# Kernel tuning notes

Hardware: AMD Instinct MI355X
Metric: run time of the kernel (lower is better)

The kernel has to match this reference:

```python
import jax, jax.numpy as jnp
import numpy as np

B = 512; NPG = 50; N = B * NPG          # graphs, nodes per graph, total nodes
EPG = 100; E = B * EPG                   # edges per graph, total edges
SPG = 5; S = B * SPG                     # stems per graph, total stems
DIM = 64; FEAT = 24
CONV_STEPS = 12; S2S_STEPS = 3; NSTEM = 105

lrelu = jax.nn.leaky_relu  # negative_slope 0.01, matches nn.LeakyReLU default

def _lin(k, o, i):
    s = 1.0 / np.sqrt(i)
    return jax.random.uniform(k, (o, i), jnp.float32, -s, s)

def _vec(k, o, i):
    s = 1.0 / np.sqrt(i)
    return jax.random.uniform(k, (o,), jnp.float32, -s, s)

def setup_inputs():
    ks = jax.random.split(jax.random.key(0), 30)
    x = jax.random.normal(ks[0], (N, FEAT), jnp.float32)
    edge_attr = jax.random.uniform(ks[1], (E, 4), jnp.float32)
    gid = jnp.arange(E) // EPG
    src = gid * NPG + jax.random.randint(ks[2], (E,), 0, NPG)
    dst = gid * NPG + jax.random.randint(ks[3], (E,), 0, NPG)
    edge_index = jnp.stack([src, dst]).astype(jnp.int32)
    batch = (jnp.arange(N) // NPG).astype(jnp.int32)
    stems = jax.random.randint(ks[4], (S,), 0, NPG).astype(jnp.int32)
    stems_batch = (jnp.arange(S) // SPG).astype(jnp.int32)
    p = dict(
        lin0_w=_lin(ks[5], DIM, FEAT), lin0_b=_vec(ks[6], DIM, FEAT),
        net1_w=_lin(ks[7], 128, 4), net1_b=_vec(ks[8], 128, 4),
        net2_w=_lin(ks[9], DIM * DIM, 128), net2_b=_vec(ks[10], DIM * DIM, 128),
        root_w=_lin(ks[11], DIM, DIM), conv_b=_vec(ks[12], DIM, DIM),
        gru_wih=_lin(ks[13], 3 * DIM, DIM), gru_whh=_lin(ks[14], 3 * DIM, DIM),
        gru_bih=_vec(ks[15], 3 * DIM, DIM), gru_bhh=_vec(ks[16], 3 * DIM, DIM),
        lin1_w=_lin(ks[17], 8 * DIM, DIM), lin1_b=_vec(ks[18], 8 * DIM, DIM),
        lin2_w=_lin(ks[19], NSTEM, 8 * DIM), lin2_b=_vec(ks[20], NSTEM, 8 * DIM),
        lstm_wih=_lin(ks[21], 4 * DIM, 2 * DIM), lstm_whh=_lin(ks[22], 4 * DIM, DIM),
        lstm_bih=_vec(ks[23], 4 * DIM, 2 * DIM), lstm_bhh=_vec(ks[24], 4 * DIM, DIM),
        lin3_w=_lin(ks[25], 1, 2 * DIM), lin3_b=_vec(ks[26], 1, 2 * DIM),
    )
    return dict(x=x, edge_attr=edge_attr, edge_index=edge_index, batch=batch,
                stems=stems, stems_batch=stems_batch, **p)

def reference(x, edge_attr, edge_index, batch, stems, stems_batch,
              lin0_w, lin0_b, net1_w, net1_b, net2_w, net2_b, root_w, conv_b,
              gru_wih, gru_whh, gru_bih, gru_bhh, lin1_w, lin1_b, lin2_w, lin2_b,
              lstm_wih, lstm_whh, lstm_bih, lstm_bhh, lin3_w, lin3_b):
    src, dst = edge_index[0], edge_index[1]
    out = lrelu(x @ lin0_w.T + lin0_b)        # [N, DIM]
    h = out                                   # GRU hidden state
    # edge-conditioned NNConv weights; edge_attr is constant across the 12 steps,
    # so the edge MLP is evaluated once (same math as re-evaluating per step)
    eh = lrelu(edge_attr @ net1_w.T + net1_b)
    W_e = (eh @ net2_w.T + net2_b).reshape(E, DIM, DIM)  # [E, DIM, DIM]
    deg = jax.ops.segment_sum(jnp.ones(E, x.dtype), dst, num_segments=N)
    inv_deg = (1.0 / jnp.maximum(deg, 1.0))[:, None]
    for _ in range(CONV_STEPS):
        msg = jnp.einsum('ed,edo->eo', out[src], W_e)               # gather + per-edge matvec
        agg = jax.ops.segment_sum(msg, dst, num_segments=N) * inv_deg  # scatter-mean
        m = lrelu(agg + out @ root_w + conv_b)                       # NNConv root + bias
        # single GRU step (torch gate order: r, z, n)
        gi = m @ gru_wih.T + gru_bih
        gh = h @ gru_whh.T + gru_bhh
        r = jax.nn.sigmoid(gi[:, :DIM] + gh[:, :DIM])
        z = jax.nn.sigmoid(gi[:, DIM:2 * DIM] + gh[:, DIM:2 * DIM])
        n = jnp.tanh(gi[:, 2 * DIM:] + r * gh[:, 2 * DIM:])
        h = (1.0 - z) * n + z * h
        out = h
    # per-stem head: data.__slices__['x'][stems_batch] + stems with uniform graphs
    stem_idx = stems_batch * NPG + stems
    stem_x = out[stem_idx]
    per_stem = lrelu(stem_x @ lin1_w.T + lin1_b) @ lin2_w.T + lin2_b  # [S, NSTEM]
    # Set2Set pooling: 3 LSTM-attention steps
    q_star = jnp.zeros((B, 2 * DIM), x.dtype)
    hs = jnp.zeros((B, DIM), x.dtype)
    cs = jnp.zeros((B, DIM), x.dtype)
    for _ in range(S2S_STEPS):
        g = q_star @ lstm_wih.T + lstm_bih + hs @ lstm_whh.T + lstm_bhh
        i_g = jax.nn.sigmoid(g[:, :DIM]); f_g = jax.nn.sigmoid(g[:, DIM:2 * DIM])
        c_g = jnp.tanh(g[:, 2 * DIM:3 * DIM]); o_g = jax.nn.sigmoid(g[:, 3 * DIM:])
        cs = f_g * cs + i_g * c_g
        hs = o_g * jnp.tanh(cs)
        e = jnp.sum(out * hs[batch], axis=-1)                        # [N]
        emax = jax.ops.segment_max(e, batch, num_segments=B)
        a = jnp.exp(e - emax[batch])
        a = a / jax.ops.segment_sum(a, batch, num_segments=B)[batch]  # segment softmax
        r_read = jax.ops.segment_sum(a[:, None] * out, batch, num_segments=B)
        q_star = jnp.concatenate([hs, r_read], axis=1)
    sout = q_star @ lin3_w.T + lin3_b   # [B, 1]
    return (per_stem, sout)
```

## Files before the change

### kernel.cpp

```cpp
#include <hip/hip_runtime.h>
#include <hip/hip_bf16.h>
#include <stdint.h>

#define N_NODES 25600
#define N_EDGES 51200
#define NG      512
#define XSTR    76

typedef __attribute__((ext_vector_type(4))) float f32x4;
typedef __attribute__((ext_vector_type(2))) float f32x2;
typedef __attribute__((ext_vector_type(8))) short bf16x8;

__device__ __forceinline__ float lrelu(float v){ return v > 0.f ? v : 0.01f*v; }
__device__ __forceinline__ float sigm(float v){ return 1.f/(1.f+__expf(-v)); }
__device__ __forceinline__ unsigned short f2b(float v){
  union { float f; uint32_t u; } x; x.f = v;
  uint32_t u = x.u;
  return (unsigned short)((u + 0x7FFFu + ((u>>16)&1u)) >> 16);
}
__device__ __forceinline__ unsigned int pk2(float a, float b){
  unsigned int r;
  asm("v_cvt_pk_bf16_f32 %0, %1, %2" : "=v"(r) : "v"(a), "v"(b));
  return r;
}
__device__ __forceinline__ float rl(float v, int l){
  return __int_as_float(__builtin_amdgcn_readlane(__float_as_int(v), l));
}

__global__ void k_prep(const float* __restrict__ net2_w, unsigned short* __restrict__ W2bT,
                       const float* __restrict__ gwih, const float* __restrict__ gwhh,
                       float* __restrict__ gw6,
                       const float* __restrict__ lwih, const float* __restrict__ lwhh,
                       float* __restrict__ lwihT, float* __restrict__ lwhhT,
                       const float* __restrict__ lin1w, float* __restrict__ l1T,
                       const float* __restrict__ lin2w, float* __restrict__ l2T,
                       const float* __restrict__ lin0w, float* __restrict__ l0T) {
  const int total = 524288+32768+32768+16384+32768+53760+1536;
  for (int i = blockIdx.x*blockDim.x + threadIdx.x; i < total; i += gridDim.x*blockDim.x) {
    int idx = i;
    if (idx < 524288) {
      int o = idx >> 13, rem = idx & 8191;
      int c = rem >> 7, r2 = rem & 127;
      int d = r2 >> 1, kl = r2 & 1;
      W2bT[idx] = f2b(net2_w[(d*64+o)*128 + (c*2+kl)]);
      continue;
    }
    idx -= 524288;
    if (idx < 32768) {
      int dt = idx >> 3, j = idx & 7;
      int d = dt >> 6, t = dt & 63;
      float v = 0.f;
      if (j < 3) v = gwih[(j*64+t)*64 + d];
      else if (j < 6) v = gwhh[((j-3)*64+t)*64 + d];
      gw6[idx] = v; continue;
    }
    idx -= 32768;
    if (idx < 32768) { int c = idx/256, j = idx%256; lwihT[idx] = lwih[j*128+c]; continue; }
    idx -= 32768;
    if (idx < 16384) { int d = idx/256, j = idx%256; lwhhT[idx] = lwhh[j*64+d]; continue; }
    idx -= 16384;
    if (idx < 32768) { int d = idx/512, j = idx%512; l1T[idx] = lin1w[j*64+d]; continue; }
    idx -= 32768;
    if (idx < 53760) { int j = idx/105, o = idx%105; l2T[idx] = lin2w[o*512+j]; continue; }
    idx -= 53760;
    { int f = idx/64, o = idx%64; l0T[idx] = lin0w[o*24+f]; }
  }
}

__global__ __launch_bounds__(256) void k_lin0(const float* __restrict__ x, const float* __restrict__ l0T,
     const float* __restrict__ b, const float* __restrict__ net2_b,
     float* __restrict__ outf, float* __restrict__ Q) {
  int t = threadIdx.x & 63;
  int n = blockIdx.x*4 + (threadIdx.x>>6);
  float xv = (t < 24) ? x[n*24+t] : 0.f;
  float acc = b[t];
  #pragma unroll
  for (int f = 0; f < 24; ++f) acc += __shfl(xv, f) * l0T[f*64+t];
  acc = lrelu(acc);
  outf[n*64+t] = acc;
  float qa = 0.f;
  #pragma unroll 8
  for (int d = 0; d < 64; ++d) qa += __shfl(acc, d) * net2_b[d*64+t];
  Q[n*64+t] = qa;
}

__global__ __launch_bounds__(256) void k_eh(const float* __restrict__ ea, const float* __restrict__ w,
    const float* __restrict__ b, float* __restrict__ ehT) {
  __shared__ float tile[128][65];
  int e0 = blockIdx.x*64;
  int tid = threadIdx.x;
  #pragma unroll
  for (int r = 0; r < 32; ++r) {
    int idx = tid + r*256; int el = idx >> 7, k = idx & 127;
    float4 a = *(const float4*)(ea + (size_t)(e0+el)*4);
    float4 ww = *(const float4*)(w + k*4);
    tile[k][el] = lrelu(a.x*ww.x + a.y*ww.y + a.z*ww.z + a.w*ww.w + b[k]);
  }
  __syncthreads();
  #pragma unroll
  for (int r = 0; r < 32; ++r) {
    int idx = tid + r*256; int k = idx >> 6, el = idx & 63;
    ehT[(size_t)k*N_EDGES + e0 + el] = tile[k][el];
  }
}

__global__ __launch_bounds__(128) void k_csr(const int* __restrict__ ei, int* __restrict__ deg,
                                             int* __restrict__ off, int* __restrict__ csr) {
  __shared__ int cnt[50];
  __shared__ int cur[50];
  __shared__ int dloc[100];
  int g = blockIdx.x, t = threadIdx.x;
  const int* dst = ei + N_EDGES;
  if (t < 50) cnt[t] = 0;
  __syncthreads();
  if (t < 100) { dloc[t] = dst[g*100+t] - g*50; atomicAdd(&cnt[dloc[t]], 1); }
  __syncthreads();
  if (t == 0) { int run = 0; for (int i = 0; i < 50; ++i) { cur[i] = run; run += cnt[i]; } }
  __syncthreads();
  if (t < 50) { deg[g*50+t] = cnt[t]; off[g*50+t] = g*100 + cur[t]; }
  __syncthreads();
  if (t < 100) {
    int p = 0, me = dloc[t];
    for (int i = 0; i < t; ++i) p += (dloc[i] == me);
    csr[g*100 + cur[me] + p] = g*100 + t;
  }
}

__global__ __launch_bounds__(512) void k_bilin(const float* __restrict__ outf,
    const float* __restrict__ ehT, const unsigned short* __restrict__ W2bT,
    const float* __restrict__ Q, const int* __restrict__ ei,
    const int* __restrict__ csr, const int* __restrict__ offs, const int* __restrict__ deg,
    float* __restrict__ agg) {
  __shared__ __align__(16) unsigned short A_lds[64*128];
  __shared__ __align__(16) unsigned short B_lds[64*128];
  __shared__ __align__(16) float xl[50*XSTR];
  __shared__ __align__(16) float ehl[256];
  __shared__ int sel[100];
  __shared__ int offl[64], degl[64];
  int tid = threadIdx.x;
  int g = blockIdx.x;
  char* Ab = (char*)A_lds;
  char* Bb = (char*)B_lds;

  if (tid < 64) {
    if (tid < 50) { offl[tid] = offs[g*50+tid] - g*100; degl[tid] = deg[g*50+tid]; }
    else { offl[tid] = 0; degl[tid] = 0; }
  }
  if (tid < 100) {
    int eg = csr[g*100 + tid];
    sel[tid] = (ei[eg] - g*50) | ((eg - g*100) << 16);
  }
  for (int i = tid; i < 3200; i += 512) xl[(i>>6)*XSTR + (i&63)] = outf[g*3200 + i];
  int sj = tid >> 1, skl = tid & 1;
  if (tid < 256 && sj < 100)
    ehl[sj*2+skl] = ehT[(size_t)skl*N_EDGES + g*100 + sj];
  int o_s = tid >> 3, j2 = tid & 7;
  int4 br0, br1;
  { const unsigned short* W2 = W2bT + (size_t)o_s*8192 + j2*16;
    br0 = *(const int4*)(W2); br1 = *(const int4*)(W2 + 8); }
  __syncthreads();

  int r = tid >> 3, dq = tid & 7, d0 = dq*8;
  int myo = offl[r], mydg = degl[r];
  uint abase = (uint)r*256u, r7 = (uint)(r & 7);
  uint bbase = (uint)o_s*256u, o7 = (uint)(o_s & 7);
  int wave = tid >> 6, lane = tid & 63;
  int nn = wave & 3, mh = wave >> 2;
  int ql = lane >> 4, cc = lane & 15;
  f32x4 acc0 = {0,0,0,0}, acc1 = {0,0,0,0};

  for (int c = 0; c < 64; ++c) {
    float ereg = 0.f;
    if (c < 63 && tid < 256 && sj < 100)
      ereg = ehT[(size_t)(2*(c+1)+skl)*N_EDGES + g*100 + sj];
    __syncthreads();
    *(int4*)(Bb + bbase + (((uint)(j2*2  ) ^ o7) << 4)) = br0;
    *(int4*)(Bb + bbase + (((uint)(j2*2+1) ^ o7) << 4)) = br1;
    if (mydg > 0) {
      f32x2 pp0 = {0,0}, pp1 = {0,0}, pp2 = {0,0}, pp3 = {0,0};
      f32x2 pp4 = {0,0}, pp5 = {0,0}, pp6 = {0,0}, pp7 = {0,0};
      for (int ii = 0; ii < mydg; ++ii) {
        int pk = sel[myo + ii];
        int s2 = pk & 0xFFFF, e2 = pk >> 16;
        f32x2 ep = *(const f32x2*)&ehl[e2*2];
        const float* xr = &xl[s2*XSTR + d0];
        float4 xa = *(const float4*)(xr);
        float4 xb = *(const float4*)(xr + 4);
        pp0 += ep * xa.x; pp1 += ep * xa.y; pp2 += ep * xa.z; pp3 += ep * xa.w;
        pp4 += ep * xb.x; pp5 += ep * xb.y; pp6 += ep * xb.z; pp7 += ep * xb.w;
      }
      int4 w0, w1;
      w0.x = pk2(pp0.x, pp0.y); w0.y = pk2(pp1.x, pp1.y);
      w0.z = pk2(pp2.x, pp2.y); w0.w = pk2(pp3.x, pp3.y);
      w1.x = pk2(pp4.x, pp4.y); w1.y = pk2(pp5.x, pp5.y);
      w1.z = pk2(pp6.x, pp6.y); w1.w = pk2(pp7.x, pp7.y);
      *(int4*)(Ab + abase + (((uint)(dq*2  ) ^ r7) << 4)) = w0;
      *(int4*)(Ab + abase + (((uint)(dq*2+1) ^ r7) << 4)) = w1;
    }
    if (c < 63) {
      const unsigned short* W2 = W2bT + (size_t)o_s*8192 + (c+1)*128 + j2*16;
      br0 = *(const int4*)(W2); br1 = *(const int4*)(W2 + 8);
    }
    __syncthreads();
    #pragma unroll
    for (int ks = 0; ks < 4; ++ks) {
      uint so = (uint)(ks*4+ql);
      bf16x8 bfr = *(const bf16x8*)(Bb + (uint)(nn*16+cc)*256u + ((so ^ (uint)((nn*16+cc)&7)) << 4));
      int rowa0 = mh*32 + cc;
      bf16x8 af0 = *(const bf16x8*)(Ab + (uint)rowa0*256u + ((so ^ (uint)(rowa0&7)) << 4));
      int rowa1 = rowa0 + 16;
      bf16x8 af1 = *(const bf16x8*)(Ab + (uint)rowa1*256u + ((so ^ (uint)(rowa1&7)) << 4));
      acc0 = __builtin_amdgcn_mfma_f32_16x16x32_bf16(af0, bfr, acc0, 0, 0, 0);
      acc1 = __builtin_amdgcn_mfma_f32_16x16x32_bf16(af1, bfr, acc1, 0, 0, 0);
    }
    if (c < 63 && tid < 256 && sj < 100) ehl[sj*2+skl] = ereg;
  }

  #pragma unroll
  for (int mi = 0; mi < 2; ++mi) {
    f32x4 a = mi ? acc1 : acc0;
    #pragma unroll
    for (int i2 = 0; i2 < 4; ++i2) {
      int v = mh*32 + mi*16 + ql*4 + i2;
      if (v < 50) {
        int o = nn*16 + cc;
        float val = 0.f;
        int dgv = degl[v];
        if (dgv > 0) {
          val = a[i2];
          int ov = offl[v];
          for (int ii = 0; ii < dgv; ++ii) {
            int s2 = sel[ov+ii] & 0xFFFF;
            val += Q[(size_t)(g*50 + s2)*64 + o];
          }
        }
        agg[(size_t)(g*50 + v)*64 + o] = val;
      }
    }
  }
}

__global__ __launch_bounds__(256) void k_upd(float* __restrict__ outf,
    const float* __restrict__ agg, const int* __restrict__ deg,
    const float* __restrict__ rootw, const float* __restrict__ conv_b,
    const float* __restrict__ gw6, const float* __restrict__ bih, const float* __restrict__ bhh,
    const float* __restrict__ net2_b, float* __restrict__ Q) {
  int t = threadIdx.x & 63;
  int n0 = (blockIdx.x*4 + (threadIdx.x >> 6)) * 8;
  float ot[8], m[8];
  #pragma unroll
  for (int i = 0; i < 8; ++i) ot[i] = outf[(size_t)(n0+i)*64 + t];
  #pragma unroll
  for (int i = 0; i < 8; ++i) {
    int dgi = deg[n0+i];
    m[i] = agg[(size_t)(n0+i)*64 + t] * (1.f/(float)(dgi > 0 ? dgi : 1));
  }
  for (int d = 0; d < 64; ++d) {
    float w = rootw[d*64+t];
    #pragma unroll
    for (int i = 0; i < 8; ++i) m[i] += rl(ot[i], d) * w;
  }
  float cb = conv_b[t];
  #pragma unroll
  for (int i = 0; i < 8; ++i) m[i] = lrelu(m[i] + cb);
  float air[8] = {}, aiz[8] = {}, ain[8] = {}, ahr[8] = {}, ahz[8] = {}, ahn[8] = {};
  for (int d = 0; d < 64; ++d) {
    float4 w0 = *(const float4*)&gw6[(d*64+t)*8];
    float4 w1 = *(const float4*)&gw6[(d*64+t)*8 + 4];
    #pragma unroll
    for (int i = 0; i < 8; ++i) {
      float md = rl(m[i], d), hd = rl(ot[i], d);
      air[i] += md*w0.x; aiz[i] += md*w0.y; ain[i] += md*w0.z;
      ahr[i] += hd*w0.w; ahz[i] += hd*w1.x; ahn[i] += hd*w1.y;
    }
  }
  float bi0 = bih[t], bi1 = bih[64+t], bi2 = bih[128+t];
  float bh0 = bhh[t], bh1 = bhh[64+t], bh2 = bhh[128+t];
  float h[8];
  #pragma unroll
  for (int i = 0; i < 8; ++i) {
    float rg = sigm(air[i] + bi0 + ahr[i] + bh0);
    float zg = sigm(aiz[i] + bi1 + ahz[i] + bh1);
    float ng = tanhf(ain[i] + bi2 + rg*(ahn[i] + bh2));
    h[i] = (1.f - zg)*ng + zg*ot[i];
    outf[(size_t)(n0+i)*64 + t] = h[i];
  }
  float qa[8] = {};
  for (int d = 0; d < 64; ++d) {
    float qw = net2_b[d*64+t];
    #pragma unroll
    for (int i = 0; i < 8; ++i) qa[i] += rl(h[i], d) * qw;
  }
  #pragma unroll
  for (int i = 0; i < 8; ++i) Q[(size_t)(n0+i)*64 + t] = qa[i];
}

__global__ __launch_bounds__(256) void k_stem(const float* __restrict__ outf,
    const int* __restrict__ stems, const int* __restrict__ stems_batch,
    const float* __restrict__ l1T, const float* __restrict__ l1b,
    const float* __restrict__ l2T, const float* __restrict__ l2b,
    float* __restrict__ per_stem) {
  int t = threadIdx.x & 63;
  int s = blockIdx.x*4 + (threadIdx.x>>6);
  int node = stems_batch[s]*50 + stems[s];
  float sx = outf[node*64+t];
  float t1[8];
  #pragma unroll
  for (int g = 0; g < 8; ++g) t1[g] = l1b[g*64+t];
  for (int d = 0; d < 64; ++d) {
    float xd = __shfl(sx, d);
    const float* L = l1T + d*512 + t;
    #pragma unroll
    for (int g = 0; g < 8; ++g) t1[g] += xd * L[g*64];
  }
  #pragma unroll
  for (int g = 0; g < 8; ++g) t1[g] = lrelu(t1[g]);
  float a0 = l2b[t];
  float a1 = (t < 41) ? l2b[64+t] : 0.f;
  for (int g = 0; g < 8; ++g) {
    for (int d = 0; d < 64; ++d) {
      float tj = __shfl(t1[g], d);
      int j = g*64 + d;
      a0 += tj * l2T[j*105 + t];
      a1 += tj * ((t < 41) ? l2T[j*105 + 64 + t] : 0.f);
    }
  }
  per_stem[s*105 + t] = a0;
  if (t < 41) per_stem[s*105 + 64 + t] = a1;
}

__global__ __launch_bounds__(64) void k_s2s(const float* __restrict__ outf,
    const float* __restrict__ wihT, const float* __restrict__ whhT,
    const float* __restrict__ bih, const float* __restrict__ bhh,
    const float* __restrict__ l3w, const float* __restrict__ l3b,
    float* __restrict__ sout) {
  int b = blockIdx.x, t = threadIdx.x;
  const float* og = outf + b*50*64;
  float qlo = 0.f, qhi = 0.f, hs = 0.f, cs = 0.f;
  float b0 = bih[t]+bhh[t], b1 = bih[64+t]+bhh[64+t], b2 = bih[128+t]+bhh[128+t], b3 = bih[192+t]+bhh[192+t];
  for (int it = 0; it < 3; ++it) {
    float g0 = b0, g1 = b1, g2 = b2, g3 = b3;
    for (int c = 0; c < 64; ++c) {
      float qc = __shfl(qlo, c);
      const float* L = wihT + c*256 + t;
      g0 += qc*L[0]; g1 += qc*L[64]; g2 += qc*L[128]; g3 += qc*L[192];
    }
    for (int c = 0; c < 64; ++c) {
      float qc = __shfl(qhi, c);
      const float* L = wihT + (64+c)*256 + t;
      g0 += qc*L[0]; g1 += qc*L[64]; g2 += qc*L[128]; g3 += qc*L[192];
    }
    for (int d = 0; d < 64; ++d) {
      float hd = __shfl(hs, d);
      const float* L = whhT + d*256 + t;
      g0 += hd*L[0]; g1 += hd*L[64]; g2 += hd*L[128]; g3 += hd*L[192];
    }
    float ig = sigm(g0), fg = sigm(g1), cg = tanhf(g2), oo = sigm(g3);
    cs = fg*cs + ig*cg;
    hs = oo*tanhf(cs);
    float ei = -3.4e38f;
    for (int i = 0; i < 50; ++i) {
      float p = og[i*64+t]*hs;
      #pragma unroll
      for (int m2 = 1; m2 < 64; m2 <<= 1) p += __shfl_xor(p, m2);
      if (t == i) ei = p;
    }
    float em = ei;
    #pragma unroll
    for (int m2 = 1; m2 < 64; m2 <<= 1) em = fmaxf(em, __shfl_xor(em, m2));
    float av = (t < 50) ? __expf(ei - em) : 0.f;
    float as = av;
    #pragma unroll
    for (int m2 = 1; m2 < 64; m2 <<= 1) as += __shfl_xor(as, m2);
    av /= as;
    float rr = 0.f;
    for (int i = 0; i < 50; ++i) rr += __shfl(av, i) * og[i*64+t];
    qlo = hs; qhi = rr;
  }
  float p = qlo*l3w[t] + qhi*l3w[64+t];
  #pragma unroll
  for (int m2 = 1; m2 < 64; m2 <<= 1) p += __shfl_xor(p, m2);
  if (t == 0) sout[b] = p + l3b[0];
}

extern "C" void kernel_launch(void* const* d_in, const int* in_sizes, int n_in,
                              void* d_out, int out_size, void* d_ws, size_t ws_size,
                              hipStream_t stream) {
  const float* x          = (const float*)d_in[0];
  const float* edge_attr  = (const float*)d_in[1];
  const int*   edge_index = (const int*)  d_in[2];
  const int*   stems      = (const int*)  d_in[4];
  const int*   stems_b    = (const int*)  d_in[5];
  const float* lin0_w = (const float*)d_in[6];
  const float* lin0_b = (const float*)d_in[7];
  const float* net1_w = (const float*)d_in[8];
  const float* net1_b = (const float*)d_in[9];
  const float* net2_w = (const float*)d_in[10];
  const float* net2_b = (const float*)d_in[11];
  const float* root_w = (const float*)d_in[12];
  const float* conv_b = (const float*)d_in[13];
  const float* gru_wih = (const float*)d_in[14];
  const float* gru_whh = (const float*)d_in[15];
  const float* gru_bih = (const float*)d_in[16];
  const float* gru_bhh = (const float*)d_in[17];
  const float* lin1_w = (const float*)d_in[18];
  const float* lin1_b = (const float*)d_in[19];
  const float* lin2_w = (const float*)d_in[20];
  const float* lin2_b = (const float*)d_in[21];
  const float* lstm_wih = (const float*)d_in[22];
  const float* lstm_whh = (const float*)d_in[23];
  const float* lstm_bih = (const float*)d_in[24];
  const float* lstm_bhh = (const float*)d_in[25];
  const float* lin3_w = (const float*)d_in[26];
  const float* lin3_b = (const float*)d_in[27];

  char* ws = (char*)d_ws;
  size_t off = 0;
  auto alloc = [&](size_t bytes) { void* p = ws + off; off += (bytes + 255) & ~(size_t)255; return p; };
  float* ehT  = (float*)alloc((size_t)N_EDGES*128*4);
  unsigned short* W2bT = (unsigned short*)alloc(524288*2);
  float* outf = (float*)alloc((size_t)N_NODES*64*4);
  float* agg  = (float*)alloc((size_t)N_NODES*64*4);
  float* Qb   = (float*)alloc((size_t)N_NODES*64*4);
  int* deg  = (int*)alloc(N_NODES*4);
  int* offs = (int*)alloc(N_NODES*4);
  int* csr  = (int*)alloc(N_EDGES*4);
  float* gw6   = (float*)alloc(32768*4);
  float* lwihT = (float*)alloc(32768*4);
  float* lwhhT = (float*)alloc(16384*4);
  float* l1T   = (float*)alloc(32768*4);
  float* l2T   = (float*)alloc(53760*4);
  float* l0T   = (float*)alloc(1536*4);

  if (off > ws_size) {
    hipMemsetAsync(d_out, 0, (size_t)out_size * sizeof(float), stream);
    return;
  }

  float* per_stem = (float*)d_out;
  float* sout = per_stem + 2560*105;

  k_prep<<<2712, 256, 0, stream>>>(net2_w, W2bT, gru_wih, gru_whh, gw6,
                                   lstm_wih, lstm_whh, lwihT, lwhhT,
                                   lin1_w, l1T, lin2_w, l2T, lin0_w, l0T);
  k_lin0<<<N_NODES/4, 256, 0, stream>>>(x, l0T, lin0_b, net2_b, outf, Qb);
  k_eh<<<N_EDGES/64, 256, 0, stream>>>(edge_attr, net1_w, net1_b, ehT);
  k_csr<<<NG, 128, 0, stream>>>(edge_index, deg, offs, csr);
  for (int s = 0; s < 12; ++s) {
    k_bilin<<<NG, 512, 0, stream>>>(outf, ehT, W2bT, Qb, edge_index, csr, offs, deg, agg);
    k_upd<<<N_NODES/32, 256, 0, stream>>>(outf, agg, deg, root_w, conv_b,
                                          gw6, gru_bih, gru_bhh, net2_b, Qb);
  }
  k_stem<<<2560/4, 256, 0, stream>>>(outf, stems, stems_b, l1T, lin1_b, l2T, lin2_b, per_stem);
  k_s2s<<<NG, 64, 0, stream>>>(outf, lwihT, lwhhT, lstm_bih, lstm_bhh, lin3_w, lin3_b, sout);
}
```

Baseline: 2.622 ms.

## Reassociate NNConv edge bilinear as node transform then gather, fuse GRU update

Reorders the NNConv message computation. Each graph's node features (in bf16) are first multiplied by the net2 weight slice for each hidden channel pair using MFMA. The per-edge scalars then scale and gather these transformed rows, replacing the old scheme that built edge-weighted node sums and then ran an MFMA against W2. The root/GRU/Q update kernel is fused into the same per-graph kernel, which removes the agg buffer round trip and one launch per step. The trade-offs are that node features are now rounded to bf16 instead of the edge-weighted sums, and the fused kernel uses more LDS and registers per block.

```diff
diff --git a/kernel.cpp b/kernel.cpp
--- a/kernel.cpp
+++ b/kernel.cpp
@@ -5,7 +5,6 @@
 #define N_NODES 25600
 #define N_EDGES 51200
 #define NG      512
-#define XSTR    76
 
 typedef __attribute__((ext_vector_type(4))) float f32x4;
 typedef __attribute__((ext_vector_type(2))) float f32x2;
@@ -18,16 +17,11 @@
   uint32_t u = x.u;
   return (unsigned short)((u + 0x7FFFu + ((u>>16)&1u)) >> 16);
 }
-__device__ __forceinline__ unsigned int pk2(float a, float b){
-  unsigned int r;
-  asm("v_cvt_pk_bf16_f32 %0, %1, %2" : "=v"(r) : "v"(a), "v"(b));
-  return r;
-}
 __device__ __forceinline__ float rl(float v, int l){
   return __int_as_float(__builtin_amdgcn_readlane(__float_as_int(v), l));
 }
 
-__global__ void k_prep(const float* __restrict__ net2_w, unsigned short* __restrict__ W2bT,
+__global__ void k_prep(const float* __restrict__ net2_w, unsigned short* __restrict__ W2n,
                        const float* __restrict__ gwih, const float* __restrict__ gwhh,
                        float* __restrict__ gw6,
                        const float* __restrict__ lwih, const float* __restrict__ lwhh,
@@ -39,10 +33,9 @@
   for (int i = blockIdx.x*blockDim.x + threadIdx.x; i < total; i += gridDim.x*blockDim.x) {
     int idx = i;
     if (idx < 524288) {
-      int o = idx >> 13, rem = idx & 8191;
-      int c = rem >> 7, r2 = rem & 127;
-      int d = r2 >> 1, kl = r2 & 1;
-      W2bT[idx] = f2b(net2_w[(d*64+o)*128 + (c*2+kl)]);
+      int n = idx >> 6, d = idx & 63;
+      int k = n >> 6, o = n & 63;
+      W2n[idx] = f2b(net2_w[(d*64+o)*128 + k]);
       continue;
     }
     idx -= 524288;
@@ -126,173 +119,215 @@
   }
 }
 
-__global__ __launch_bounds__(512) void k_bilin(const float* __restrict__ outf,
-    const float* __restrict__ ehT, const unsigned short* __restrict__ W2bT,
-    const float* __restrict__ Q, const int* __restrict__ ei,
-    const int* __restrict__ csr, const int* __restrict__ offs, const int* __restrict__ deg,
-    float* __restrict__ agg) {
-  __shared__ __align__(16) unsigned short A_lds[64*128];
-  __shared__ __align__(16) unsigned short B_lds[64*128];
-  __shared__ __align__(16) float xl[50*XSTR];
-  __shared__ __align__(16) float ehl[256];
+__global__ __launch_bounds__(512, 4) void k_step(
+    float* __restrict__ outf, const float* __restrict__ ehT,
+    const unsigned short* __restrict__ W2n, float* __restrict__ Qb,
+    const int* __restrict__ ei, const int* __restrict__ csr,
+    const int* __restrict__ offs, const int* __restrict__ deg,
+    const float* __restrict__ rootw, const float* __restrict__ conv_b,
+    const float* __restrict__ gw6, const float* __restrict__ bih, const float* __restrict__ bhh,
+    const float* __restrict__ net2_b) {
+  __shared__ __align__(16) char  BtB[128*144];
+  __shared__ __align__(16) float Tt[64*132];
+  __shared__ __align__(16) char  XbB[64*144];
+  __shared__ float ehl[2][256];
   __shared__ int sel[100];
-  __shared__ int offl[64], degl[64];
-  int tid = threadIdx.x;
-  int g = blockIdx.x;
-  char* Ab = (char*)A_lds;
-  char* Bb = (char*)B_lds;
+  __shared__ int offl[64];
+  __shared__ int degl[64];
+  __shared__ float invd[64];
+  float* aggL = (float*)BtB;
+
+  const int tid = threadIdx.x;
+  const int g = blockIdx.x;
+  const int wave = tid >> 6, lane = tid & 63;
+  const int t = lane;
+  const int q = lane >> 4, cc = lane & 15;
+  const int mw = wave >> 1, nh = wave & 1;
 
   if (tid < 64) {
-    if (tid < 50) { offl[tid] = offs[g*50+tid] - g*100; degl[tid] = deg[g*50+tid]; }
-    else { offl[tid] = 0; degl[tid] = 0; }
+    int dgv = 0, ofv = 0;
+    if (tid < 50) { dgv = deg[g*50+tid]; ofv = offs[g*50+tid] - g*100; }
+    degl[tid] = dgv; offl[tid] = ofv;
+    invd[tid] = 1.f/(float)(dgv > 0 ? dgv : 1);
   }
   if (tid < 100) {
-    int eg = csr[g*100 + tid];
-    sel[tid] = (ei[eg] - g*50) | ((eg - g*100) << 16);
-  }
-  for (int i = tid; i < 3200; i += 512) xl[(i>>6)*XSTR + (i&63)] = outf[g*3200 + i];
-  int sj = tid >> 1, skl = tid & 1;
-  if (tid < 256 && sj < 100)
-    ehl[sj*2+skl] = ehT[(size_t)skl*N_EDGES + g*100 + sj];
-  int o_s = tid >> 3, j2 = tid & 7;
+    int eg = csr[g*100+tid];
+    sel[tid] = (ei[eg]-g*50) | ((eg-g*100) << 16);
+  }
+  for (int i = tid; i < 64*72; i += 512) ((unsigned short*)XbB)[i] = 0;
+  __syncthreads();
+  for (int i = tid; i < 3200; i += 512) {
+    int n = i >> 6, d = i & 63;
+    ((unsigned short*)XbB)[n*72+d] = f2b(outf[(size_t)g*3200 + i]);
+  }
+  __syncthreads();
+
+  bf16x8 xf00, xf01, xf10, xf11;
+  {
+    int xr0 = nh*32 + cc, xr1 = xr0 + 16;
+    xf00 = *(const bf16x8*)(XbB + xr0*144 + (q*8)*2);
+    xf01 = *(const bf16x8*)(XbB + xr0*144 + (32+q*8)*2);
+    xf10 = *(const bf16x8*)(XbB + xr1*144 + (q*8)*2);
+    xf11 = *(const bf16x8*)(XbB + xr1*144 + (32+q*8)*2);
+  }
+
+  const int r = tid >> 3, dq = tid & 7;
+  const int myo = offl[r], mydg = degl[r];
+  const float* ehTg = ehT + (size_t)g*100;
+  const int brow = tid >> 2, bpart = tid & 3;
+
   int4 br0, br1;
-  { const unsigned short* W2 = W2bT + (size_t)o_s*8192 + j2*16;
-    br0 = *(const int4*)(W2); br1 = *(const int4*)(W2 + 8); }
-  __syncthreads();
-
-  int r = tid >> 3, dq = tid & 7, d0 = dq*8;
-  int myo = offl[r], mydg = degl[r];
-  uint abase = (uint)r*256u, r7 = (uint)(r & 7);
-  uint bbase = (uint)o_s*256u, o7 = (uint)(o_s & 7);
-  int wave = tid >> 6, lane = tid & 63;
-  int nn = wave & 3, mh = wave >> 2;
-  int ql = lane >> 4, cc = lane & 15;
-  f32x4 acc0 = {0,0,0,0}, acc1 = {0,0,0,0};
-
+  {
+    const unsigned short* src = W2n + (size_t)brow*64 + bpart*16;
+    br0 = *(const int4*)src; br1 = *(const int4*)(src + 8);
+  }
+  float er0 = 0.f, er1 = 0.f;
+  if (tid < 100) { er0 = ehTg[0*(size_t)N_EDGES + tid]; er1 = ehTg[1*(size_t)N_EDGES + tid]; }
+  *(int4*)(BtB + brow*144 + (((bpart*2  )^(brow&7))<<4)) = br0;
+  *(int4*)(BtB + brow*144 + (((bpart*2+1)^(brow&7))<<4)) = br1;
+  if (tid < 100) { ehl[0][tid*2] = er0; ehl[0][tid*2+1] = er1; }
+  __syncthreads();
+
+  float fin0=0.f, fin1=0.f, fin2=0.f, fin3=0.f, fin4=0.f, fin5=0.f, fin6=0.f, fin7=0.f;
+
+  #pragma unroll 1
   for (int c = 0; c < 64; ++c) {
-    float ereg = 0.f;
-    if (c < 63 && tid < 256 && sj < 100)
-      ereg = ehT[(size_t)(2*(c+1)+skl)*N_EDGES + g*100 + sj];
+    f32x4 tc00={}, tc01={}, tc10={}, tc11={};
+    {
+      int ar0 = mw*32 + cc, ar1 = ar0 + 16;
+      #pragma unroll
+      for (int ks = 0; ks < 2; ++ks) {
+        bf16x8 af0 = *(const bf16x8*)(BtB + ar0*144 + (((ks*4+q)^(ar0&7))<<4));
+        bf16x8 af1 = *(const bf16x8*)(BtB + ar1*144 + (((ks*4+q)^(ar1&7))<<4));
+        bf16x8 xb0 = ks ? xf01 : xf00;
+        bf16x8 xb1 = ks ? xf11 : xf10;
+        tc00 = __builtin_amdgcn_mfma_f32_16x16x32_bf16(af0, xb0, tc00, 0,0,0);
+        tc01 = __builtin_amdgcn_mfma_f32_16x16x32_bf16(af0, xb1, tc01, 0,0,0);
+        tc10 = __builtin_amdgcn_mfma_f32_16x16x32_bf16(af1, xb0, tc10, 0,0,0);
+        tc11 = __builtin_amdgcn_mfma_f32_16x16x32_bf16(af1, xb1, tc11, 0,0,0);
+      }
+    }
+    {
+      int n0a = mw*32 + q*4, n0b = n0a + 16;
+      int sA = nh*32 + cc,   sB = sA + 16;
+      float4 v;
+      v.x=tc00[0]; v.y=tc00[1]; v.z=tc00[2]; v.w=tc00[3];
+      *(float4*)&Tt[sA*132 + n0a] = v;
+      v.x=tc01[0]; v.y=tc01[1]; v.z=tc01[2]; v.w=tc01[3];
+      *(float4*)&Tt[sB*132 + n0a] = v;
+      v.x=tc10[0]; v.y=tc10[1]; v.z=tc10[2]; v.w=tc10[3];
+      *(float4*)&Tt[sA*132 + n0b] = v;
+      v.x=tc11[0]; v.y=tc11[1]; v.z=tc11[2]; v.w=tc11[3];
+      *(float4*)&Tt[sB*132 + n0b] = v;
+    }
+    if (c < 63) {
+      const unsigned short* src = W2n + ((size_t)(c+1)*128 + brow)*64 + bpart*16;
+      br0 = *(const int4*)src; br1 = *(const int4*)(src + 8);
+      if (tid < 100) {
+        er0 = ehTg[(size_t)(2*c+2)*N_EDGES + tid];
+        er1 = ehTg[(size_t)(2*c+3)*N_EDGES + tid];
+      }
+    }
     __syncthreads();
-    *(int4*)(Bb + bbase + (((uint)(j2*2  ) ^ o7) << 4)) = br0;
-    *(int4*)(Bb + bbase + (((uint)(j2*2+1) ^ o7) << 4)) = br1;
-    if (mydg > 0) {
-      f32x2 pp0 = {0,0}, pp1 = {0,0}, pp2 = {0,0}, pp3 = {0,0};
-      f32x2 pp4 = {0,0}, pp5 = {0,0}, pp6 = {0,0}, pp7 = {0,0};
+    {
+      const float* ebuf = ehl[c & 1];
       for (int ii = 0; ii < mydg; ++ii) {
         int pk = sel[myo + ii];
-        int s2 = pk & 0xFFFF, e2 = pk >> 16;
-        f32x2 ep = *(const f32x2*)&ehl[e2*2];
-        const float* xr = &xl[s2*XSTR + d0];
-        float4 xa = *(const float4*)(xr);
-        float4 xb = *(const float4*)(xr + 4);
-        pp0 += ep * xa.x; pp1 += ep * xa.y; pp2 += ep * xa.z; pp3 += ep * xa.w;
-        pp4 += ep * xb.x; pp5 += ep * xb.y; pp6 += ep * xb.z; pp7 += ep * xb.w;
-      }
-      int4 w0, w1;
-      w0.x = pk2(pp0.x, pp0.y); w0.y = pk2(pp1.x, pp1.y);
-      w0.z = pk2(pp2.x, pp2.y); w0.w = pk2(pp3.x, pp3.y);
-      w1.x = pk2(pp4.x, pp4.y); w1.y = pk2(pp5.x, pp5.y);
-      w1.z = pk2(pp6.x, pp6.y); w1.w = pk2(pp7.x, pp7.y);
-      *(int4*)(Ab + abase + (((uint)(dq*2  ) ^ r7) << 4)) = w0;
-      *(int4*)(Ab + abase + (((uint)(dq*2+1) ^ r7) << 4)) = w1;
+        int s2 = pk & 0xffff, e2 = pk >> 16;
+        float ex = ebuf[e2*2], ey = ebuf[e2*2+1];
+        const float* tb = &Tt[s2*132];
+        float4 ta0 = *(const float4*)(tb + dq*8);
+        float4 ta1 = *(const float4*)(tb + dq*8 + 4);
+        float4 tb0 = *(const float4*)(tb + 64 + dq*8);
+        float4 tb1 = *(const float4*)(tb + 64 + dq*8 + 4);
+        fin0 += ex*ta0.x + ey*tb0.x;  fin1 += ex*ta0.y + ey*tb0.y;
+        fin2 += ex*ta0.z + ey*tb0.z;  fin3 += ex*ta0.w + ey*tb0.w;
+        fin4 += ex*ta1.x + ey*tb1.x;  fin5 += ex*ta1.y + ey*tb1.y;
+        fin6 += ex*ta1.z + ey*tb1.z;  fin7 += ex*ta1.w + ey*tb1.w;
+      }
     }
     if (c < 63) {
-      const unsigned short* W2 = W2bT + (size_t)o_s*8192 + (c+1)*128 + j2*16;
-      br0 = *(const int4*)(W2); br1 = *(const int4*)(W2 + 8);
+      *(int4*)(BtB + brow*144 + (((bpart*2  )^(brow&7))<<4)) = br0;
+      *(int4*)(BtB + brow*144 + (((bpart*2+1)^(brow&7))<<4)) = br1;
+      if (tid < 100) { ehl[(c+1)&1][tid*2] = er0; ehl[(c+1)&1][tid*2+1] = er1; }
     }
     __syncthreads();
-    #pragma unroll
-    for (int ks = 0; ks < 4; ++ks) {
-      uint so = (uint)(ks*4+ql);
-      bf16x8 bfr = *(const bf16x8*)(Bb + (uint)(nn*16+cc)*256u + ((so ^ (uint)((nn*16+cc)&7)) << 4));
-      int rowa0 = mh*32 + cc;
-      bf16x8 af0 = *(const bf16x8*)(Ab + (uint)rowa0*256u + ((so ^ (uint)(rowa0&7)) << 4));
-      int rowa1 = rowa0 + 16;
-      bf16x8 af1 = *(const bf16x8*)(Ab + (uint)rowa1*256u + ((so ^ (uint)(rowa1&7)) << 4));
-      acc0 = __builtin_amdgcn_mfma_f32_16x16x32_bf16(af0, bfr, acc0, 0, 0, 0);
-      acc1 = __builtin_amdgcn_mfma_f32_16x16x32_bf16(af1, bfr, acc1, 0, 0, 0);
-    }
-    if (c < 63 && tid < 256 && sj < 100) ehl[sj*2+skl] = ereg;
-  }
-
-  #pragma unroll
-  for (int mi = 0; mi < 2; ++mi) {
-    f32x4 a = mi ? acc1 : acc0;
-    #pragma unroll
-    for (int i2 = 0; i2 < 4; ++i2) {
-      int v = mh*32 + mi*16 + ql*4 + i2;
-      if (v < 50) {
-        int o = nn*16 + cc;
-        float val = 0.f;
-        int dgv = degl[v];
-        if (dgv > 0) {
-          val = a[i2];
-          int ov = offl[v];
-          for (int ii = 0; ii < dgv; ++ii) {
-            int s2 = sel[ov+ii] & 0xFFFF;
-            val += Q[(size_t)(g*50 + s2)*64 + o];
-          }
-        }
-        agg[(size_t)(g*50 + v)*64 + o] = val;
-      }
-    }
-  }
-}
-
-__global__ __launch_bounds__(256) void k_upd(float* __restrict__ outf,
-    const float* __restrict__ agg, const int* __restrict__ deg,
-    const float* __restrict__ rootw, const float* __restrict__ conv_b,
-    const float* __restrict__ gw6, const float* __restrict__ bih, const float* __restrict__ bhh,
-    const float* __restrict__ net2_b, float* __restrict__ Q) {
-  int t = threadIdx.x & 63;
-  int n0 = (blockIdx.x*4 + (threadIdx.x >> 6)) * 8;
-  float ot[8], m[8];
-  #pragma unroll
-  for (int i = 0; i < 8; ++i) ot[i] = outf[(size_t)(n0+i)*64 + t];
-  #pragma unroll
-  for (int i = 0; i < 8; ++i) {
-    int dgi = deg[n0+i];
-    m[i] = agg[(size_t)(n0+i)*64 + t] * (1.f/(float)(dgi > 0 ? dgi : 1));
-  }
-  for (int d = 0; d < 64; ++d) {
-    float w = rootw[d*64+t];
-    #pragma unroll
-    for (int i = 0; i < 8; ++i) m[i] += rl(ot[i], d) * w;
-  }
-  float cb = conv_b[t];
-  #pragma unroll
-  for (int i = 0; i < 8; ++i) m[i] = lrelu(m[i] + cb);
-  float air[8] = {}, aiz[8] = {}, ain[8] = {}, ahr[8] = {}, ahz[8] = {}, ahn[8] = {};
-  for (int d = 0; d < 64; ++d) {
-    float4 w0 = *(const float4*)&gw6[(d*64+t)*8];
-    float4 w1 = *(const float4*)&gw6[(d*64+t)*8 + 4];
+  }
+
+  {
+    for (int ii = 0; ii < mydg; ++ii) {
+      int s2 = sel[myo + ii] & 0xffff;
+      const float* qp = Qb + (size_t)(g*50 + s2)*64 + dq*8;
+      float4 q0 = *(const float4*)(qp);
+      float4 q1 = *(const float4*)(qp + 4);
+      fin0 += q0.x; fin1 += q0.y; fin2 += q0.z; fin3 += q0.w;
+      fin4 += q1.x; fin5 += q1.y; fin6 += q1.z; fin7 += q1.w;
+    }
+    float4 f0 = {fin0, fin1, fin2, fin3};
+    float4 f1 = {fin4, fin5, fin6, fin7};
+    *(float4*)&aggL[r*66 + dq*8]     = f0;
+    *(float4*)&aggL[r*66 + dq*8 + 4] = f1;
+  }
+  __syncthreads();
+
+  {
+    float ot[8];
     #pragma unroll
     for (int i = 0; i < 8; ++i) {
-      float md = rl(m[i], d), hd = rl(ot[i], d);
-      air[i] += md*w0.x; aiz[i] += md*w0.y; ain[i] += md*w0.z;
-      ahr[i] += hd*w0.w; ahz[i] += hd*w1.x; ahn[i] += hd*w1.y;
-    }
-  }
-  float bi0 = bih[t], bi1 = bih[64+t], bi2 = bih[128+t];
-  float bh0 = bhh[t], bh1 = bhh[64+t], bh2 = bhh[128+t];
-  float h[8];
-  #pragma unroll
-  for (int i = 0; i < 8; ++i) {
-    float rg = sigm(air[i] + bi0 + ahr[i] + bh0);
-    float zg = sigm(aiz[i] + bi1 + ahz[i] + bh1);
-    float ng = tanhf(ain[i] + bi2 + rg*(ahn[i] + bh2));
-    h[i] = (1.f - zg)*ng + zg*ot[i];
-    outf[(size_t)(n0+i)*64 + t] = h[i];
-  }
-  float qa[8] = {};
-  for (int d = 0; d < 64; ++d) {
-    float qw = net2_b[d*64+t];
-    #pragma unroll
-    for (int i = 0; i < 8; ++i) qa[i] += rl(h[i], d) * qw;
-  }
-  #pragma unroll
-  for (int i = 0; i < 8; ++i) Q[(size_t)(n0+i)*64 + t] = qa[i];
+      int n = wave*8 + i;
+      ot[i] = (n < 50) ? outf[(size_t)(g*50+n)*64 + t] : 0.f;
+    }
+    float mm[8];
+    {
+      float rc[8] = {0,0,0,0,0,0,0,0};
+      for (int d = 0; d < 64; ++d) {
+        float w = rootw[d*64+t];
+        #pragma unroll
+        for (int i = 0; i < 8; ++i) rc[i] += rl(ot[i], d) * w;
+      }
+      float cb = conv_b[t];
+      #pragma unroll
+      for (int i = 0; i < 8; ++i) {
+        int n = wave*8 + i;
+        mm[i] = lrelu(aggL[n*66 + t]*invd[n] + rc[i] + cb);
+      }
+    }
+    float air[8]={}, aiz[8]={}, ain[8]={}, ahr[8]={}, ahz[8]={}, ahn[8]={};
+    for (int d = 0; d < 64; ++d) {
+      const float* wp = gw6 + (size_t)(d*64+t)*8;
+      float4 w0 = *(const float4*)wp;
+      float4 w1 = *(const float4*)(wp + 4);
+      #pragma unroll
+      for (int i = 0; i < 8; ++i) {
+        float md = rl(mm[i], d), hd = rl(ot[i], d);
+        air[i] += md*w0.x; aiz[i] += md*w0.y; ain[i] += md*w0.z;
+        ahr[i] += hd*w0.w; ahz[i] += hd*w1.x; ahn[i] += hd*w1.y;
+      }
+    }
+    float bi0 = bih[t], bi1 = bih[64+t], bi2 = bih[128+t];
+    float bh0 = bhh[t], bh1 = bhh[64+t], bh2 = bhh[128+t];
+    float h[8];
+    #pragma unroll
+    for (int i = 0; i < 8; ++i) {
+      int n = wave*8 + i;
+      float rg = sigm(air[i] + bi0 + ahr[i] + bh0);
+      float zg = sigm(aiz[i] + bi1 + ahz[i] + bh1);
+      float ng = tanhf(ain[i] + bi2 + rg*(ahn[i] + bh2));
+      h[i] = (1.f - zg)*ng + zg*ot[i];
+      if (n < 50) outf[(size_t)(g*50+n)*64 + t] = h[i];
+    }
+    float qa[8] = {0,0,0,0,0,0,0,0};
+    for (int d = 0; d < 64; ++d) {
+      float qw = net2_b[d*64+t];
+      #pragma unroll
+      for (int i = 0; i < 8; ++i) qa[i] += rl(h[i], d) * qw;
+    }
+    #pragma unroll
+    for (int i = 0; i < 8; ++i) {
+      int n = wave*8 + i;
+      if (n < 50) Qb[(size_t)(g*50+n)*64 + t] = qa[i];
+    }
+  }
 }
 
 __global__ __launch_bounds__(256) void k_stem(const float* __restrict__ outf,
@@ -418,9 +453,8 @@
   size_t off = 0;
   auto alloc = [&](size_t bytes) { void* p = ws + off; off += (bytes + 255) & ~(size_t)255; return p; };
   float* ehT  = (float*)alloc((size_t)N_EDGES*128*4);
-  unsigned short* W2bT = (unsigned short*)alloc(524288*2);
+  unsigned short* W2n = (unsigned short*)alloc(524288*2);
   float* outf = (float*)alloc((size_t)N_NODES*64*4);
-  float* agg  = (float*)alloc((size_t)N_NODES*64*4);
   float* Qb   = (float*)alloc((size_t)N_NODES*64*4);
   int* deg  = (int*)alloc(N_NODES*4);
   int* offs = (int*)alloc(N_NODES*4);
@@ -440,16 +474,15 @@
   float* per_stem = (float*)d_out;
   float* sout = per_stem + 2560*105;
 
-  k_prep<<<2712, 256, 0, stream>>>(net2_w, W2bT, gru_wih, gru_whh, gw6,
+  k_prep<<<2712, 256, 0, stream>>>(net2_w, W2n, gru_wih, gru_whh, gw6,
                                    lstm_wih, lstm_whh, lwihT, lwhhT,
                                    lin1_w, l1T, lin2_w, l2T, lin0_w, l0T);
   k_lin0<<<N_NODES/4, 256, 0, stream>>>(x, l0T, lin0_b, net2_b, outf, Qb);
   k_eh<<<N_EDGES/64, 256, 0, stream>>>(edge_attr, net1_w, net1_b, ehT);
   k_csr<<<NG, 128, 0, stream>>>(edge_index, deg, offs, csr);
   for (int s = 0; s < 12; ++s) {
-    k_bilin<<<NG, 512, 0, stream>>>(outf, ehT, W2bT, Qb, edge_index, csr, offs, deg, agg);
-    k_upd<<<N_NODES/32, 256, 0, stream>>>(outf, agg, deg, root_w, conv_b,
-                                          gw6, gru_bih, gru_bhh, net2_b, Qb);
+    k_step<<<NG, 512, 0, stream>>>(outf, ehT, W2n, Qb, edge_index, csr, offs, deg,
+                                   root_w, conv_b, gw6, gru_bih, gru_bhh, net2_b);
   }
   k_stem<<<2560/4, 256, 0, stream>>>(outf, stems, stems_b, l1T, lin1_b, l2T, lin2_b, per_stem);
   k_s2s<<<NG, 64, 0, stream>>>(outf, lwihT, lwhhT, lstm_bih, lstm_bhh, lin3_w, lin3_b, sout);
```

New measurement: 2.795 ms. +6.6%, slower.
